# Performance work log

Measured on AMD Instinct MI355X. Metric: run time of the kernel, lower is better.

The kernel has to match this reference:

```python
import jax, jax.numpy as jnp
import numpy as np

S, B, C, H = 8192, 4, 512, 8
D = C // H
EPS = 1e-6


def setup_inputs() -> dict:
    key = jax.random.key(0)
    ks = jax.random.split(key, 11)
    scale = 1.0 / np.sqrt(C)
    return {
        "query": jax.random.normal(ks[0], (S, B, C), jnp.float32),
        "key": jax.random.normal(ks[1], (S, B, C), jnp.float32),
        "value": jax.random.normal(ks[2], (S, B, C), jnp.float32),
        "Wq": jax.random.normal(ks[3], (C, C), jnp.float32) * scale,
        "bq": jnp.zeros((C,), jnp.float32),
        "Wk": jax.random.normal(ks[4], (C, C), jnp.float32) * scale,
        "bk": jnp.zeros((C,), jnp.float32),
        "Wv": jax.random.normal(ks[5], (C, C), jnp.float32) * scale,
        "bv": jnp.zeros((C,), jnp.float32),
        "Wp": jax.random.normal(ks[6], (C, C), jnp.float32) * scale,
        "bp": jnp.zeros((C,), jnp.float32),
    }


def _elu_fm(x):
    # ELU(x) + 1 feature map
    return jax.nn.elu(x) + 1.0


def _heads(x, W, b):
    # x: [B, N, C] -> [B, H, N, D]
    y = x @ W.T + b
    Bb, N, _ = y.shape
    return y.reshape(Bb, N, H, D).transpose(0, 2, 1, 3)


def reference(query, key, value, Wq, bq, Wk, bk, Wv, bv, Wp, bp):
    # inputs [S, B, C] -> batch-first [B, S, C]
    q_in = query.transpose(1, 0, 2)
    k_in = key.transpose(1, 0, 2)
    v_in = value.transpose(1, 0, 2)

    q = _elu_fm(_heads(q_in, Wq, bq))   # [B,H,N,D]
    k = _elu_fm(_heads(k_in, Wk, bk))   # [B,H,N,D]
    v = _heads(v_in, Wv, bv)            # [B,H,N,D]

    # linear attention: O(N) kv-sum formulation
    kv = jnp.einsum('bhnd,bhnf->bhdf', k, v)       # [B,H,D,D]
    k_sum = k.sum(axis=2)                          # [B,H,D]
    qkv = jnp.einsum('bhnd,bhdf->bhnf', q, kv)     # [B,H,N,D]
    denom = jnp.einsum('bhnd,bhd->bhn', q, k_sum)  # [B,H,N]
    y = qkv / (denom[..., None] + EPS)

    # merge heads, output projection, back to [S, B, C]
    y = y.transpose(0, 2, 1, 3).reshape(q_in.shape[0], q_in.shape[1], C)
    out = y @ Wp.T + bp
    return out.transpose(1, 0, 2)
```

## Files before the change

kernel.cpp:

```cpp
#include <hip/hip_runtime.h>
#include <hip/hip_bf16.h>
#include <math.h>

#define S_LEN 8192
#define BATCH 4
#define CDIM  512
#define HEADS 8
#define DDIM  64
#define MROWS (S_LEN * BATCH)
#define EPS_F 1e-6f

typedef __attribute__((ext_vector_type(8))) short     short8_t;
typedef __attribute__((ext_vector_type(4))) float     f32x4;
typedef unsigned short ushort_t;
typedef __attribute__((ext_vector_type(4))) unsigned short ushort4_t;
typedef __attribute__((ext_vector_type(8))) unsigned short ushort8_t;

static __device__ __forceinline__ ushort_t f2bf(float f) {
  __hip_bfloat16 h = __float2bfloat16(f);
  return *(ushort_t*)&h;
}

static __device__ __forceinline__ void gl2lds16(const ushort_t* g, ushort_t* l) {
  __builtin_amdgcn_global_load_lds((const __attribute__((address_space(1))) void*)g,
                                   (__attribute__((address_space(3))) void*)l,
                                   16, 0, 0);
}

__global__ __launch_bounds__(256)
void cvtW_pack(const float* __restrict__ a, const float* __restrict__ b,
               const float* __restrict__ c, const float* __restrict__ d,
               ushort_t* __restrict__ oa, ushort_t* __restrict__ ob,
               ushort_t* __restrict__ oc, ushort_t* __restrict__ od) {
  const float* src = (blockIdx.y == 0) ? a : (blockIdx.y == 1) ? b :
                     (blockIdx.y == 2) ? c : d;
  ushort_t* dst    = (blockIdx.y == 0) ? oa : (blockIdx.y == 1) ? ob :
                     (blockIdx.y == 2) ? oc : od;
  const size_t i = ((size_t)blockIdx.x * 256 + threadIdx.x) * 8;
  const int n  = (int)(i >> 9);
  const int k0 = (int)(i & 511);
  const float4 x = *(const float4*)&src[i];
  const float4 y = *(const float4*)&src[i + 4];
  ushort8_t p;
  p[0] = f2bf(x.x); p[1] = f2bf(x.y); p[2] = f2bf(x.z); p[3] = f2bf(x.w);
  p[4] = f2bf(y.x); p[5] = f2bf(y.y); p[6] = f2bf(y.z); p[7] = f2bf(y.w);
  const int kf   = k0 >> 5;
  const int lane = ((k0 >> 3) & 3) * 16 + (n & 15);
  const int nfg  = n >> 4;
  *(ushort8_t*)&dst[(((size_t)nfg * 16 + kf) * 64 + lane) * 8] = p;
}

template<int OUTF32>
static __device__ __forceinline__
void nobar_compute(const ushort_t* __restrict__ alds,
                   const ushort_t* __restrict__ Wpk,
                   const float* __restrict__ bias, void* __restrict__ Yv,
                   const bool act, const int m0) {
  const int t    = threadIdx.x;
  const int w    = t >> 6;
  const int lane = t & 63;

  f32x4 acc[4][8];
  #pragma unroll
  for (int mi = 0; mi < 4; ++mi)
    #pragma unroll
    for (int nf = 0; nf < 8; ++nf)
      acc[mi][nf] = (f32x4){0.f, 0.f, 0.f, 0.f};

  short8_t a_[4], b0[8], b1[8];

  auto LB = [&](int kf, short8_t (&bb)[8]) {
    #pragma unroll
    for (int nf = 0; nf < 8; ++nf)
      bb[nf] = *(const short8_t*)&Wpk[(((size_t)(w * 8 + nf) * 16 + kf) * 64 + lane) * 8];
  };
  auto LA = [&](int kf) {
    #pragma unroll
    for (int mi = 0; mi < 4; ++mi)
      a_[mi] = *(const short8_t*)&alds[((kf * 4 + mi) * 64 + lane) * 8];
  };
  auto MF = [&](short8_t (&bb)[8]) {
    #pragma unroll
    for (int mi = 0; mi < 4; ++mi)
      #pragma unroll
      for (int nf = 0; nf < 8; ++nf)
        acc[mi][nf] = __builtin_amdgcn_mfma_f32_16x16x32_bf16(
            a_[mi], bb[nf], acc[mi][nf], 0, 0, 0);
  };

  LB(0, b0);
  #pragma unroll
  for (int kk = 0; kk < 8; ++kk) {
    LB(kk * 2 + 1, b1);
    LA(kk * 2);
    MF(b0);
    if (kk < 7) LB(kk * 2 + 2, b0);
    LA(kk * 2 + 1);
    MF(b1);
  }

  float* Yf = (float*)Yv;
  ushort_t* Yh = (ushort_t*)Yv;
  #pragma unroll
  for (int nf = 0; nf < 8; ++nf) {
    const int col = w * 128 + nf * 16 + (lane & 15);
    const float bi = bias[col];
    #pragma unroll
    for (int mi = 0; mi < 4; ++mi) {
      #pragma unroll
      for (int r = 0; r < 4; ++r) {
        const int m = m0 + mi * 16 + (lane >> 4) * 4 + r;
        float vv = acc[mi][nf][r] + bi;
        if (act) vv = (vv > 0.f) ? (vv + 1.f) : expf(vv);
        if (OUTF32) Yf[(size_t)m * CDIM + col] = vv;
        else        Yh[(size_t)m * CDIM + col] = f2bf(vv);
      }
    }
  }
}

__global__ __launch_bounds__(256)
void proj3_nobar(const float* __restrict__ Xq, const float* __restrict__ Xk,
                 const float* __restrict__ Xv,
                 const ushort_t* __restrict__ Wqp, const ushort_t* __restrict__ Wkp,
                 const ushort_t* __restrict__ Wvp,
                 const float* __restrict__ bq, const float* __restrict__ bk,
                 const float* __restrict__ bv,
                 ushort_t* __restrict__ Yq, ushort_t* __restrict__ Yk,
                 ushort_t* __restrict__ Yv) {
  __shared__ __align__(16) ushort_t alds[32768];
  const int z = blockIdx.y;
  const float*    X    = (z == 0) ? Xq : (z == 1) ? Xk : Xv;
  const ushort_t* Wpk  = (z == 0) ? Wqp : (z == 1) ? Wkp : Wvp;
  const float*    bias = (z == 0) ? bq : (z == 1) ? bk : bv;
  ushort_t*       Y    = (z == 0) ? Yq : (z == 1) ? Yk : Yv;
  const int t  = threadIdx.x;
  const int m0 = blockIdx.x * 64;

  #pragma unroll
  for (int it = 0; it < 16; ++it) {
    const int u   = it * 256 + t;
    const int row = u >> 6;
    const int k8  = u & 63;
    const float4 x0 = *(const float4*)&X[(size_t)(m0 + row) * CDIM + k8 * 8];
    const float4 x1 = *(const float4*)&X[(size_t)(m0 + row) * CDIM + k8 * 8 + 4];
    short8_t v;
    v[0] = (short)f2bf(x0.x); v[1] = (short)f2bf(x0.y);
    v[2] = (short)f2bf(x0.z); v[3] = (short)f2bf(x0.w);
    v[4] = (short)f2bf(x1.x); v[5] = (short)f2bf(x1.y);
    v[6] = (short)f2bf(x1.z); v[7] = (short)f2bf(x1.w);
    const int kf = k8 >> 2, mf = row >> 4;
    const int ln = (k8 & 3) * 16 + (row & 15);
    *(short8_t*)&alds[((kf * 4 + mf) * 64 + ln) * 8] = v;
  }
  __syncthreads();

  nobar_compute<0>(alds, Wpk, bias, Y, z < 2, m0);
}

__global__ __launch_bounds__(256)
void outp_nobar(const ushort_t* __restrict__ A, const ushort_t* __restrict__ Wpk,
                const float* __restrict__ bias, float* __restrict__ Y) {
  __shared__ __align__(16) ushort_t alds[32768];
  const int t    = threadIdx.x;
  const int w    = t >> 6;
  const int lane = t & 63;
  const int m0   = blockIdx.x * 64;

  #pragma unroll
  for (int j = 0; j < 16; ++j) {
    const int fid = w * 16 + j;
    const int kf = fid >> 2, mf = fid & 3;
    const ushort_t* ga = A +
        (size_t)(m0 + mf * 16 + (lane & 15)) * CDIM + kf * 32 + (lane >> 4) * 8;
    gl2lds16(ga, (ushort_t*)&alds[fid * 512]);
  }
  __syncthreads();

  nobar_compute<1>(alds, Wpk, bias, Y, false, m0);
}

__global__ __launch_bounds__(256)
void gemm_kv(const ushort_t* __restrict__ Kb, const ushort_t* __restrict__ Vb,
             float* __restrict__ kvpart, float* __restrict__ ksumpart) {
  __shared__ __align__(16) ushort_t klds[8192];
  __shared__ __align__(16) ushort_t vlds[8192];
  const int bh    = blockIdx.x;
  const int chunk = blockIdx.y;
  const int b = bh >> 3, h = bh & 7;
  const int t = threadIdx.x;
  const int w = t >> 6;
  const int lane = t & 63;

  f32x4 acc[4];
  #pragma unroll
  for (int fg = 0; fg < 4; ++fg) acc[fg] = (f32x4){0.f, 0.f, 0.f, 0.f};
  f32x4 accs = (f32x4){0.f, 0.f, 0.f, 0.f};

  short8_t ones;
  #pragma unroll
  for (int i = 0; i < 8; ++i) ones[i] = (short)0x3F80;

  for (int round = 0; round < 4; ++round) {
    const int sbase = chunk * 512 + round * 128;
    __syncthreads();
    #pragma unroll
    for (int i = 0; i < 4; ++i) {
      const int idx  = i * 256 + t;
      const int sl   = idx >> 3;
      const int d8   = idx & 7;
      const size_t src = (size_t)((sbase + sl) * BATCH + b) * CDIM + h * DDIM + d8 * 8;
      const ushort8_t kp = *(const ushort8_t*)&Kb[src];
      const ushort8_t vp = *(const ushort8_t*)&Vb[src];
      const int sb  = sl >> 5;
      const int j   = sl & 7;
      const int lp0 = (d8 & 1) * 8 + ((sl >> 3) & 3) * 16;
      const int dg  = d8 >> 1;
      const int kbase = ((sb * 4 + dg) * 64 + lp0) * 8 + j;
      #pragma unroll
      for (int e = 0; e < 8; ++e) {
        klds[kbase + e * 8] = kp[e];
        vlds[kbase + e * 8] = vp[e];
      }
    }
    __syncthreads();
    #pragma unroll
    for (int sb = 0; sb < 4; ++sb) {
      const short8_t af = *(const short8_t*)&klds[((sb * 4 + w) * 64 + lane) * 8];
      accs = __builtin_amdgcn_mfma_f32_16x16x32_bf16(af, ones, accs, 0, 0, 0);
      #pragma unroll
      for (int fg = 0; fg < 4; ++fg) {
        const short8_t bf = *(const short8_t*)&vlds[((sb * 4 + fg) * 64 + lane) * 8];
        acc[fg] = __builtin_amdgcn_mfma_f32_16x16x32_bf16(af, bf, acc[fg], 0, 0, 0);
      }
    }
  }

  const size_t obase = ((size_t)bh * 16 + chunk) * 64;
  #pragma unroll
  for (int fg = 0; fg < 4; ++fg)
    #pragma unroll
    for (int r = 0; r < 4; ++r) {
      const int d = w * 16 + (lane >> 4) * 4 + r;
      kvpart[(obase + d) * 64 + fg * 16 + (lane & 15)] = acc[fg][r];
    }
  if ((lane & 15) == 0) {
    #pragma unroll
    for (int r = 0; r < 4; ++r)
      ksumpart[obase + w * 16 + (lane >> 4) * 4 + r] = accs[r];
  }
}

__global__ __launch_bounds__(256)
void kv_finish(const float* __restrict__ kvpart, const float* __restrict__ ksumpart,
               ushort_t* __restrict__ kvT) {
  const int bh = blockIdx.x;
  const int t  = threadIdx.x;
  for (int idx = t; idx < 4096; idx += 256) {
    const int d = idx >> 6, f = idx & 63;
    float s = 0.f;
    for (int c = 0; c < 16; ++c)
      s += kvpart[(((size_t)bh * 16 + c) * 64 + d) * 64 + f];
    kvT[((size_t)bh * 80 + f) * 64 + d] = f2bf(s);
  }
  if (t < 64) {
    float s = 0.f;
    for (int c = 0; c < 16; ++c)
      s += ksumpart[((size_t)bh * 16 + c) * 64 + t];
    kvT[((size_t)bh * 80 + 64) * 64 + t] = f2bf(s);
  }
  for (int i = t; i < 15 * 64; i += 256)
    kvT[((size_t)bh * 80 + 65) * 64 + i] = 0;
}

__global__ __launch_bounds__(256)
void gemm_qkv(ushort_t* __restrict__ Qb, const ushort_t* __restrict__ kvT) {
  __shared__ __align__(16) ushort_t alds[8192];
  __shared__ __align__(16) ushort_t blds[5120];
  const int bh    = blockIdx.x;
  const int chunk = blockIdx.y;
  const int b = bh >> 3, h = bh & 7;
  const int t = threadIdx.x;
  const int w = t >> 6;
  const int lane = t & 63;
  const int lr = lane & 15;
  const int lk = (lane >> 4) * 8;

  #pragma unroll
  for (int i = 0; i < 4; ++i) {
    const int fidx = w * 4 + i;
    const int ks = fidx >> 3, fm = fidx & 7;
    const ushort_t* src = Qb +
        (size_t)((chunk * 128 + fm * 16 + lr) * BATCH + b) * CDIM +
        h * DDIM + ks * 32 + lk;
    gl2lds16(src, &alds[fidx * 512]);
  }
  for (int idx = w; idx < 10; idx += 4) {
    const int ks = idx / 5, fg = idx % 5;
    const ushort_t* src = kvT + (size_t)(bh * 80 + fg * 16 + lr) * 64 + ks * 32 + lk;
    gl2lds16(src, &blds[idx * 512]);
  }
  __syncthreads();

  f32x4 acc[2][5];
  #pragma unroll
  for (int mi = 0; mi < 2; ++mi)
    #pragma unroll
    for (int fg = 0; fg < 5; ++fg)
      acc[mi][fg] = (f32x4){0.f, 0.f, 0.f, 0.f};

  #pragma unroll
  for (int ks = 0; ks < 2; ++ks) {
    short8_t af[2], bf[5];
    #pragma unroll
    for (int mi = 0; mi < 2; ++mi)
      af[mi] = *(const short8_t*)&alds[(ks * 8 + w * 2 + mi) * 512 + lane * 8];
    #pragma unroll
    for (int fg = 0; fg < 5; ++fg)
      bf[fg] = *(const short8_t*)&blds[(ks * 5 + fg) * 512 + lane * 8];
    #pragma unroll
    for (int mi = 0; mi < 2; ++mi)
      #pragma unroll
      for (int fg = 0; fg < 5; ++fg)
        acc[mi][fg] = __builtin_amdgcn_mfma_f32_16x16x32_bf16(
            af[mi], bf[fg], acc[mi][fg], 0, 0, 0);
  }

  #pragma unroll
  for (int mi = 0; mi < 2; ++mi) {
    #pragma unroll
    for (int r = 0; r < 4; ++r) {
      const float dv  = __shfl(acc[mi][4][r], lane & 48);
      const float inv = 1.f / (dv + EPS_F);
      const int s = chunk * 128 + w * 32 + mi * 16 + (lane >> 4) * 4 + r;
      const size_t rowb = (size_t)(s * BATCH + b) * CDIM + h * DDIM;
      #pragma unroll
      for (int fg = 0; fg < 4; ++fg)
        Qb[rowb + fg * 16 + lr] = f2bf(acc[mi][fg][r] * inv);
    }
  }
}

extern "C" void kernel_launch(void* const* d_in, const int* in_sizes, int n_in,
                              void* d_out, int out_size, void* d_ws, size_t ws_size,
                              hipStream_t stream) {
  const float* q_in = (const float*)d_in[0];
  const float* k_in = (const float*)d_in[1];
  const float* v_in = (const float*)d_in[2];
  const float* Wq   = (const float*)d_in[3];
  const float* bq   = (const float*)d_in[4];
  const float* Wk   = (const float*)d_in[5];
  const float* bk   = (const float*)d_in[6];
  const float* Wv   = (const float*)d_in[7];
  const float* bv   = (const float*)d_in[8];
  const float* Wp   = (const float*)d_in[9];
  const float* bp   = (const float*)d_in[10];
  float* out = (float*)d_out;

  const size_t NTOK = (size_t)MROWS * CDIM;
  const size_t NW   = (size_t)CDIM * CDIM;
  ushort_t* Wqp    = (ushort_t*)d_ws;
  ushort_t* Wkp    = Wqp + NW;
  ushort_t* Wvp    = Wkp + NW;
  ushort_t* Wpp    = Wvp + NW;
  ushort_t* qbuf   = Wpp + NW;
  ushort_t* kbuf   = qbuf + NTOK;
  ushort_t* vbuf   = kbuf + NTOK;
  ushort_t* kvT    = vbuf + NTOK;
  float* kvpart    = (float*)(kvT + (size_t)32 * 80 * 64);
  float* ksumpart  = kvpart + (size_t)512 * 64 * 64;

  const dim3 blk(256);

  cvtW_pack<<<dim3(128, 4), blk, 0, stream>>>(Wq, Wk, Wv, Wp,
                                              Wqp, Wkp, Wvp, Wpp);

  proj3_nobar<<<dim3(MROWS / 64, 3), blk, 0, stream>>>(
      q_in, k_in, v_in, Wqp, Wkp, Wvp, bq, bk, bv, qbuf, kbuf, vbuf);

  gemm_kv<<<dim3(32, 16), blk, 0, stream>>>(kbuf, vbuf, kvpart, ksumpart);
  kv_finish<<<dim3(32), blk, 0, stream>>>(kvpart, ksumpart, kvT);

  gemm_qkv<<<dim3(32, 64), blk, 0, stream>>>(qbuf, kvT);

  outp_nobar<<<dim3(MROWS / 64), blk, 0, stream>>>(qbuf, Wpp, bp, out);
}
```

Before: 234.4 us.

## Stage projection outputs through LDS for coalesced stores and use nontemporal loads/stores

The QKV projection kernel now writes its bf16 results into shared memory first and then copies them to global memory as contiguous 16-byte rows, replacing the scattered 2-byte stores. It also reads the fp32 inputs with a fragment-aligned pattern using nontemporal loads. The output projection uses nontemporal stores. The GEMM main loop is restructured so the B-fragment prefetch runs two k-steps ahead. The extra barriers and the LDS round trip add latency, and the input reads per wave become less contiguous in exchange for simpler LDS writes.

```diff
diff --git a/kernel.cpp b/kernel.cpp
--- a/kernel.cpp
+++ b/kernel.cpp
@@ -50,17 +50,10 @@
   *(ushort8_t*)&dst[(((size_t)nfg * 16 + kf) * 64 + lane) * 8] = p;
 }
 
-template<int OUTF32>
 static __device__ __forceinline__
-void nobar_compute(const ushort_t* __restrict__ alds,
-                   const ushort_t* __restrict__ Wpk,
-                   const float* __restrict__ bias, void* __restrict__ Yv,
-                   const bool act, const int m0) {
-  const int t    = threadIdx.x;
-  const int w    = t >> 6;
-  const int lane = t & 63;
-
-  f32x4 acc[4][8];
+void nobar_mainloop(const ushort_t* __restrict__ alds,
+                    const ushort_t* __restrict__ Wpk,
+                    const int w, const int lane, f32x4 (&acc)[4][8]) {
   #pragma unroll
   for (int mi = 0; mi < 4; ++mi)
     #pragma unroll
@@ -89,32 +82,16 @@
   };
 
   LB(0, b0);
-  #pragma unroll
-  for (int kk = 0; kk < 8; ++kk) {
-    LB(kk * 2 + 1, b1);
-    LA(kk * 2);
-    MF(b0);
-    if (kk < 7) LB(kk * 2 + 2, b0);
-    LA(kk * 2 + 1);
-    MF(b1);
-  }
-
-  float* Yf = (float*)Yv;
-  ushort_t* Yh = (ushort_t*)Yv;
-  #pragma unroll
-  for (int nf = 0; nf < 8; ++nf) {
-    const int col = w * 128 + nf * 16 + (lane & 15);
-    const float bi = bias[col];
-    #pragma unroll
-    for (int mi = 0; mi < 4; ++mi) {
-      #pragma unroll
-      for (int r = 0; r < 4; ++r) {
-        const int m = m0 + mi * 16 + (lane >> 4) * 4 + r;
-        float vv = acc[mi][nf][r] + bi;
-        if (act) vv = (vv > 0.f) ? (vv + 1.f) : expf(vv);
-        if (OUTF32) Yf[(size_t)m * CDIM + col] = vv;
-        else        Yh[(size_t)m * CDIM + col] = f2bf(vv);
-      }
+  LB(1, b1);
+  #pragma unroll
+  for (int kk = 0; kk < 16; ++kk) {
+    LA(kk);
+    if (kk & 1) {
+      MF(b1);
+      if (kk + 2 < 16) LB(kk + 2, b1);
+    } else {
+      MF(b0);
+      if (kk + 2 < 16) LB(kk + 2, b0);
     }
   }
 }
@@ -134,28 +111,55 @@
   const ushort_t* Wpk  = (z == 0) ? Wqp : (z == 1) ? Wkp : Wvp;
   const float*    bias = (z == 0) ? bq : (z == 1) ? bk : bv;
   ushort_t*       Y    = (z == 0) ? Yq : (z == 1) ? Yk : Yv;
-  const int t  = threadIdx.x;
-  const int m0 = blockIdx.x * 64;
-
+  const int t    = threadIdx.x;
+  const int w    = t >> 6;
+  const int lane = t & 63;
+  const int r15  = lane & 15;
+  const int kwin = lane >> 4;
+  const int m0   = blockIdx.x * 64;
+
+  const float* abase = X + (size_t)(m0 + w * 16 + r15) * CDIM + kwin * 8;
+  #pragma unroll
+  for (int it = 0; it < 16; ++it) {
+    const f32x4 x0 = __builtin_nontemporal_load((const f32x4*)(abase + it * 32));
+    const f32x4 x1 = __builtin_nontemporal_load((const f32x4*)(abase + it * 32 + 4));
+    short8_t v;
+    v[0] = (short)f2bf(x0[0]); v[1] = (short)f2bf(x0[1]);
+    v[2] = (short)f2bf(x0[2]); v[3] = (short)f2bf(x0[3]);
+    v[4] = (short)f2bf(x1[0]); v[5] = (short)f2bf(x1[1]);
+    v[6] = (short)f2bf(x1[2]); v[7] = (short)f2bf(x1[3]);
+    *(short8_t*)&alds[((it * 4 + w) * 64 + lane) * 8] = v;
+  }
+  __syncthreads();
+
+  f32x4 acc[4][8];
+  nobar_mainloop(alds, Wpk, w, lane, acc);
+
+  __syncthreads();
+  const bool act = (z < 2);
+  #pragma unroll
+  for (int nf = 0; nf < 8; ++nf) {
+    const int col = w * 128 + nf * 16 + r15;
+    const float bi = bias[col];
+    #pragma unroll
+    for (int mi = 0; mi < 4; ++mi)
+      #pragma unroll
+      for (int r = 0; r < 4; ++r) {
+        const int row = mi * 16 + kwin * 4 + r;
+        float vv = acc[mi][nf][r] + bi;
+        if (act) vv = (vv > 0.f) ? (vv + 1.f) : expf(vv);
+        alds[row * 512 + col] = f2bf(vv);
+      }
+  }
+  __syncthreads();
   #pragma unroll
   for (int it = 0; it < 16; ++it) {
     const int u   = it * 256 + t;
     const int row = u >> 6;
-    const int k8  = u & 63;
-    const float4 x0 = *(const float4*)&X[(size_t)(m0 + row) * CDIM + k8 * 8];
-    const float4 x1 = *(const float4*)&X[(size_t)(m0 + row) * CDIM + k8 * 8 + 4];
-    short8_t v;
-    v[0] = (short)f2bf(x0.x); v[1] = (short)f2bf(x0.y);
-    v[2] = (short)f2bf(x0.z); v[3] = (short)f2bf(x0.w);
-    v[4] = (short)f2bf(x1.x); v[5] = (short)f2bf(x1.y);
-    v[6] = (short)f2bf(x1.z); v[7] = (short)f2bf(x1.w);
-    const int kf = k8 >> 2, mf = row >> 4;
-    const int ln = (k8 & 3) * 16 + (row & 15);
-    *(short8_t*)&alds[((kf * 4 + mf) * 64 + ln) * 8] = v;
-  }
-  __syncthreads();
-
-  nobar_compute<0>(alds, Wpk, bias, Y, z < 2, m0);
+    const int c8  = (u & 63) * 8;
+    const short8_t v = *(const short8_t*)&alds[u * 8];
+    __builtin_nontemporal_store(v, (short8_t*)&Y[(size_t)(m0 + row) * CDIM + c8]);
+  }
 }
 
 __global__ __launch_bounds__(256)
@@ -177,7 +181,23 @@
   }
   __syncthreads();
 
-  nobar_compute<1>(alds, Wpk, bias, Y, false, m0);
+  f32x4 acc[4][8];
+  nobar_mainloop(alds, Wpk, w, lane, acc);
+
+  #pragma unroll
+  for (int nf = 0; nf < 8; ++nf) {
+    const int col = w * 128 + nf * 16 + (lane & 15);
+    const float bi = bias[col];
+    #pragma unroll
+    for (int mi = 0; mi < 4; ++mi) {
+      #pragma unroll
+      for (int r = 0; r < 4; ++r) {
+        const int m = m0 + mi * 16 + (lane >> 4) * 4 + r;
+        __builtin_nontemporal_store(acc[mi][nf][r] + bi,
+                                    &Y[(size_t)m * CDIM + col]);
+      }
+    }
+  }
 }
 
 __global__ __launch_bounds__(256)
```

After: 247.0 us. +5.3%, slower.

## Retile projection GEMMs to 256x256 blocks with double-buffered LDS pipeline

Applied to the files above, without the earlier changes.

Replaces the 64-row full-N projection and output GEMM kernels with a shared 256x256-tile GEMM body using 512 threads. A and B tiles are double-buffered in 128KB of dynamic LDS, with register prefetch for the fp32 input path and global_load_lds for the bf16 and weight paths. The bf16 output is staged through LDS for coalesced non-temporal stores. This aims to raise reuse of weights and activations per block and to overlap loads with MFMA work. In exchange it uses heavy LDS and registers per block, which limits occupancy.

```diff
diff --git a/kernel.cpp b/kernel.cpp
--- a/kernel.cpp
+++ b/kernel.cpp
@@ -13,7 +13,6 @@
 typedef __attribute__((ext_vector_type(8))) short     short8_t;
 typedef __attribute__((ext_vector_type(4))) float     f32x4;
 typedef unsigned short ushort_t;
-typedef __attribute__((ext_vector_type(4))) unsigned short ushort4_t;
 typedef __attribute__((ext_vector_type(8))) unsigned short ushort8_t;
 
 static __device__ __forceinline__ ushort_t f2bf(float f) {
@@ -50,134 +49,203 @@
   *(ushort8_t*)&dst[(((size_t)nfg * 16 + kf) * 64 + lane) * 8] = p;
 }
 
-template<int OUTF32>
+template<int AF32, int OUTF32>
 static __device__ __forceinline__
-void nobar_compute(const ushort_t* __restrict__ alds,
-                   const ushort_t* __restrict__ Wpk,
-                   const float* __restrict__ bias, void* __restrict__ Yv,
-                   const bool act, const int m0) {
+void gemm256_body(const void* __restrict__ Av, const ushort_t* __restrict__ Wpk,
+                  const float* __restrict__ bias, void* __restrict__ Yv,
+                  const bool act, const int m0, const int n0, ushort_t* lds) {
   const int t    = threadIdx.x;
   const int w    = t >> 6;
   const int lane = t & 63;
-
-  f32x4 acc[4][8];
-  #pragma unroll
-  for (int mi = 0; mi < 4; ++mi)
-    #pragma unroll
-    for (int nf = 0; nf < 8; ++nf)
-      acc[mi][nf] = (f32x4){0.f, 0.f, 0.f, 0.f};
-
-  short8_t a_[4], b0[8], b1[8];
-
-  auto LB = [&](int kf, short8_t (&bb)[8]) {
-    #pragma unroll
-    for (int nf = 0; nf < 8; ++nf)
-      bb[nf] = *(const short8_t*)&Wpk[(((size_t)(w * 8 + nf) * 16 + kf) * 64 + lane) * 8];
+  const int lr   = lane & 15;
+  const int lk8  = (lane >> 4) * 8;
+  const int wm   = (w >> 2) * 128;
+  const int wn   = (w & 3) * 64;
+
+  const float*    Xf = (const float*)Av;
+  const ushort_t* Ah = (const ushort_t*)Av;
+
+  ushort_t* A0 = lds;
+  ushort_t* A1 = lds + 16384;
+  ushort_t* B0 = lds + 32768;
+  ushort_t* B1 = lds + 49152;
+
+  f32x4 ar[4][2];
+
+  auto regloadA = [&](int kt) {
+    #pragma unroll
+    for (int j = 0; j < 4; ++j) {
+      const int fid = w * 4 + j;
+      const size_t g = (size_t)(m0 + (fid >> 1) * 16 + lr) * CDIM +
+                       kt + (fid & 1) * 32 + lk8;
+      ar[j][0] = __builtin_nontemporal_load((const f32x4*)&Xf[g]);
+      ar[j][1] = __builtin_nontemporal_load((const f32x4*)&Xf[g + 4]);
+    }
   };
-  auto LA = [&](int kf) {
-    #pragma unroll
-    for (int mi = 0; mi < 4; ++mi)
-      a_[mi] = *(const short8_t*)&alds[((kf * 4 + mi) * 64 + lane) * 8];
+  auto stageA_f32 = [&](ushort_t* Ab) {
+    #pragma unroll
+    for (int j = 0; j < 4; ++j) {
+      const int fid = w * 4 + j;
+      short8_t v;
+      v[0] = (short)f2bf(ar[j][0][0]); v[1] = (short)f2bf(ar[j][0][1]);
+      v[2] = (short)f2bf(ar[j][0][2]); v[3] = (short)f2bf(ar[j][0][3]);
+      v[4] = (short)f2bf(ar[j][1][0]); v[5] = (short)f2bf(ar[j][1][1]);
+      v[6] = (short)f2bf(ar[j][1][2]); v[7] = (short)f2bf(ar[j][1][3]);
+      *(short8_t*)&lds[(Ab - lds) + (size_t)fid * 512 + lane * 8] = v;
+    }
   };
-  auto MF = [&](short8_t (&bb)[8]) {
-    #pragma unroll
-    for (int mi = 0; mi < 4; ++mi)
-      #pragma unroll
-      for (int nf = 0; nf < 8; ++nf)
-        acc[mi][nf] = __builtin_amdgcn_mfma_f32_16x16x32_bf16(
-            a_[mi], bb[nf], acc[mi][nf], 0, 0, 0);
+  auto stageA_bf16 = [&](ushort_t* Ab, int kt) {
+    #pragma unroll
+    for (int j = 0; j < 4; ++j) {
+      const int fid = w * 4 + j;
+      const ushort_t* g = Ah + (size_t)(m0 + (fid >> 1) * 16 + lr) * CDIM +
+                          kt + (fid & 1) * 32 + lk8;
+      gl2lds16(g, &Ab[fid * 512]);
+    }
   };
-
-  LB(0, b0);
-  #pragma unroll
-  for (int kk = 0; kk < 8; ++kk) {
-    LB(kk * 2 + 1, b1);
-    LA(kk * 2);
-    MF(b0);
-    if (kk < 7) LB(kk * 2 + 2, b0);
-    LA(kk * 2 + 1);
-    MF(b1);
-  }
-
-  float* Yf = (float*)Yv;
-  ushort_t* Yh = (ushort_t*)Yv;
-  #pragma unroll
-  for (int nf = 0; nf < 8; ++nf) {
-    const int col = w * 128 + nf * 16 + (lane & 15);
-    const float bi = bias[col];
-    #pragma unroll
-    for (int mi = 0; mi < 4; ++mi) {
-      #pragma unroll
-      for (int r = 0; r < 4; ++r) {
-        const int m = m0 + mi * 16 + (lane >> 4) * 4 + r;
-        float vv = acc[mi][nf][r] + bi;
-        if (act) vv = (vv > 0.f) ? (vv + 1.f) : expf(vv);
-        if (OUTF32) Yf[(size_t)m * CDIM + col] = vv;
-        else        Yh[(size_t)m * CDIM + col] = f2bf(vv);
-      }
-    }
-  }
-}
-
-__global__ __launch_bounds__(256)
-void proj3_nobar(const float* __restrict__ Xq, const float* __restrict__ Xk,
-                 const float* __restrict__ Xv,
-                 const ushort_t* __restrict__ Wqp, const ushort_t* __restrict__ Wkp,
-                 const ushort_t* __restrict__ Wvp,
-                 const float* __restrict__ bq, const float* __restrict__ bk,
-                 const float* __restrict__ bv,
-                 ushort_t* __restrict__ Yq, ushort_t* __restrict__ Yk,
-                 ushort_t* __restrict__ Yv) {
-  __shared__ __align__(16) ushort_t alds[32768];
-  const int z = blockIdx.y;
+  auto stageB = [&](ushort_t* Bb, int kt) {
+    #pragma unroll
+    for (int j = 0; j < 4; ++j) {
+      const int fid = w * 4 + j;
+      const size_t idx = ((size_t)((n0 >> 4) + (fid >> 1)) * 16 +
+                          (kt >> 5) + (fid & 1));
+      gl2lds16(Wpk + idx * 512 + lane * 8, &Bb[fid * 512]);
+    }
+  };
+
+  f32x4 acc[8][4];
+  #pragma unroll
+  for (int mf = 0; mf < 8; ++mf)
+    #pragma unroll
+    for (int nf = 0; nf < 4; ++nf)
+      acc[mf][nf] = (f32x4){0.f, 0.f, 0.f, 0.f};
+
+  auto compute = [&](const ushort_t* Ab, const ushort_t* Bb) {
+    short8_t bfr[2][4];
+    #pragma unroll
+    for (int kf = 0; kf < 2; ++kf)
+      #pragma unroll
+      for (int nf = 0; nf < 4; ++nf) {
+        const int fidb = ((wn >> 4) + nf) * 2 + kf;
+        bfr[kf][nf] = *(const short8_t*)&Bb[fidb * 512 + lane * 8];
+      }
+    #pragma unroll
+    for (int mf = 0; mf < 8; ++mf) {
+      const int fa = ((wm >> 4) + mf) * 2;
+      const short8_t a0 = *(const short8_t*)&Ab[(fa + 0) * 512 + lane * 8];
+      const short8_t a1 = *(const short8_t*)&Ab[(fa + 1) * 512 + lane * 8];
+      #pragma unroll
+      for (int nf = 0; nf < 4; ++nf)
+        acc[mf][nf] = __builtin_amdgcn_mfma_f32_16x16x32_bf16(
+            a0, bfr[0][nf], acc[mf][nf], 0, 0, 0);
+      #pragma unroll
+      for (int nf = 0; nf < 4; ++nf)
+        acc[mf][nf] = __builtin_amdgcn_mfma_f32_16x16x32_bf16(
+            a1, bfr[1][nf], acc[mf][nf], 0, 0, 0);
+    }
+  };
+
+  if (AF32) {
+    regloadA(0);
+    stageA_f32(A0);
+    stageB(B0, 0);
+    regloadA(64);
+  } else {
+    stageA_bf16(A0, 0);
+    stageB(B0, 0);
+  }
+  __syncthreads();
+
+  #pragma unroll
+  for (int ks = 0; ks < 8; ++ks) {
+    ushort_t* curA = (ks & 1) ? A1 : A0;
+    ushort_t* curB = (ks & 1) ? B1 : B0;
+    ushort_t* nxtA = (ks & 1) ? A0 : A1;
+    ushort_t* nxtB = (ks & 1) ? B0 : B1;
+    if (ks < 7) {
+      if (AF32) {
+        stageA_f32(nxtA);
+        if (ks + 2 < 8) regloadA((ks + 2) * 64);
+      } else {
+        stageA_bf16(nxtA, (ks + 1) * 64);
+      }
+      stageB(nxtB, (ks + 1) * 64);
+    }
+    compute(curA, curB);
+    __syncthreads();
+  }
+
+  if (OUTF32) {
+    float* Yf = (float*)Yv;
+    #pragma unroll
+    for (int nf = 0; nf < 4; ++nf) {
+      const int col = n0 + wn + nf * 16 + lr;
+      const float bi = bias[col];
+      #pragma unroll
+      for (int mf = 0; mf < 8; ++mf) {
+        #pragma unroll
+        for (int r = 0; r < 4; ++r) {
+          const int m = m0 + wm + mf * 16 + (lane >> 4) * 4 + r;
+          __builtin_nontemporal_store(acc[mf][nf][r] + bi,
+                                      &Yf[(size_t)m * CDIM + col]);
+        }
+      }
+    }
+  } else {
+    ushort_t* Yh = (ushort_t*)Yv;
+    #pragma unroll
+    for (int nf = 0; nf < 4; ++nf) {
+      const int col = wn + nf * 16 + lr;
+      const float bi = bias[n0 + col];
+      #pragma unroll
+      for (int mf = 0; mf < 8; ++mf) {
+        #pragma unroll
+        for (int r = 0; r < 4; ++r) {
+          const int row = wm + mf * 16 + (lane >> 4) * 4 + r;
+          float vv = acc[mf][nf][r] + bi;
+          if (act) vv = (vv > 0.f) ? (vv + 1.f) : expf(vv);
+          lds[row * 256 + col] = f2bf(vv);
+        }
+      }
+    }
+    __syncthreads();
+    #pragma unroll
+    for (int it = 0; it < 16; ++it) {
+      const int u   = it * 512 + t;
+      const int row = u >> 5;
+      const int c8  = (u & 31) * 8;
+      const short8_t v = *(const short8_t*)&lds[u * 8];
+      __builtin_nontemporal_store(
+          v, (short8_t*)&Yh[(size_t)(m0 + row) * CDIM + n0 + c8]);
+    }
+  }
+}
+
+__global__ __launch_bounds__(512)
+void proj3_256(const float* __restrict__ Xq, const float* __restrict__ Xk,
+               const float* __restrict__ Xv,
+               const ushort_t* __restrict__ Wqp, const ushort_t* __restrict__ Wkp,
+               const ushort_t* __restrict__ Wvp,
+               const float* __restrict__ bq, const float* __restrict__ bk,
+               const float* __restrict__ bv,
+               ushort_t* __restrict__ Yq, ushort_t* __restrict__ Yk,
+               ushort_t* __restrict__ Yv) {
+  extern __shared__ ushort_t lds[];
+  const int z = blockIdx.z;
   const float*    X    = (z == 0) ? Xq : (z == 1) ? Xk : Xv;
   const ushort_t* Wpk  = (z == 0) ? Wqp : (z == 1) ? Wkp : Wvp;
   const float*    bias = (z == 0) ? bq : (z == 1) ? bk : bv;
   ushort_t*       Y    = (z == 0) ? Yq : (z == 1) ? Yk : Yv;
-  const int t  = threadIdx.x;
-  const int m0 = blockIdx.x * 64;
-
-  #pragma unroll
-  for (int it = 0; it < 16; ++it) {
-    const int u   = it * 256 + t;
-    const int row = u >> 6;
-    const int k8  = u & 63;
-    const float4 x0 = *(const float4*)&X[(size_t)(m0 + row) * CDIM + k8 * 8];
-    const float4 x1 = *(const float4*)&X[(size_t)(m0 + row) * CDIM + k8 * 8 + 4];
-    short8_t v;
-    v[0] = (short)f2bf(x0.x); v[1] = (short)f2bf(x0.y);
-    v[2] = (short)f2bf(x0.z); v[3] = (short)f2bf(x0.w);
-    v[4] = (short)f2bf(x1.x); v[5] = (short)f2bf(x1.y);
-    v[6] = (short)f2bf(x1.z); v[7] = (short)f2bf(x1.w);
-    const int kf = k8 >> 2, mf = row >> 4;
-    const int ln = (k8 & 3) * 16 + (row & 15);
-    *(short8_t*)&alds[((kf * 4 + mf) * 64 + ln) * 8] = v;
-  }
-  __syncthreads();
-
-  nobar_compute<0>(alds, Wpk, bias, Y, z < 2, m0);
-}
-
-__global__ __launch_bounds__(256)
-void outp_nobar(const ushort_t* __restrict__ A, const ushort_t* __restrict__ Wpk,
-                const float* __restrict__ bias, float* __restrict__ Y) {
-  __shared__ __align__(16) ushort_t alds[32768];
-  const int t    = threadIdx.x;
-  const int w    = t >> 6;
-  const int lane = t & 63;
-  const int m0   = blockIdx.x * 64;
-
-  #pragma unroll
-  for (int j = 0; j < 16; ++j) {
-    const int fid = w * 16 + j;
-    const int kf = fid >> 2, mf = fid & 3;
-    const ushort_t* ga = A +
-        (size_t)(m0 + mf * 16 + (lane & 15)) * CDIM + kf * 32 + (lane >> 4) * 8;
-    gl2lds16(ga, (ushort_t*)&alds[fid * 512]);
-  }
-  __syncthreads();
-
-  nobar_compute<1>(alds, Wpk, bias, Y, false, m0);
+  gemm256_body<1, 0>(X, Wpk, bias, Y, z < 2,
+                     blockIdx.y * 256, blockIdx.x * 256, lds);
+}
+
+__global__ __launch_bounds__(512)
+void outp_256(const ushort_t* __restrict__ A, const ushort_t* __restrict__ Wpk,
+              const float* __restrict__ bias, float* __restrict__ Y) {
+  extern __shared__ ushort_t lds[];
+  gemm256_body<0, 1>(A, Wpk, bias, Y, false,
+                     blockIdx.y * 256, blockIdx.x * 256, lds);
 }
 
 __global__ __launch_bounds__(256)
@@ -371,11 +439,12 @@
   float* ksumpart  = kvpart + (size_t)512 * 64 * 64;
 
   const dim3 blk(256);
+  const size_t LDSB = 131072;
 
   cvtW_pack<<<dim3(128, 4), blk, 0, stream>>>(Wq, Wk, Wv, Wp,
                                               Wqp, Wkp, Wvp, Wpp);
 
-  proj3_nobar<<<dim3(MROWS / 64, 3), blk, 0, stream>>>(
+  proj3_256<<<dim3(CDIM / 256, MROWS / 256, 3), dim3(512), LDSB, stream>>>(
       q_in, k_in, v_in, Wqp, Wkp, Wvp, bq, bk, bv, qbuf, kbuf, vbuf);
 
   gemm_kv<<<dim3(32, 16), blk, 0, stream>>>(kbuf, vbuf, kvpart, ksumpart);
@@ -383,5 +452,6 @@
 
   gemm_qkv<<<dim3(32, 64), blk, 0, stream>>>(qbuf, kvT);
 
-  outp_nobar<<<dim3(MROWS / 64), blk, 0, stream>>>(qbuf, Wpp, bp, out);
-}
+  outp_256<<<dim3(CDIM / 256, MROWS / 256), dim3(512), LDSB, stream>>>(
+      qbuf, Wpp, bp, out);
+}
```

New measurement: 241.5 us. +3.0%, slower.
